# Performance work log

Hardware: AMD Instinct MI355X
Metric: run time of the kernel (lower is better)

Reference implementation:

```python
import jax, jax.numpy as jnp
import numpy as np
import math


def setup_inputs() -> dict:
    key = jax.random.key(0)
    kq, kk, kv = jax.random.split(key, 3)
    B, HQ, HKV, S, D = 1, 32, 8, 2048, 128
    query = jax.random.normal(kq, (B, HQ, S, D), dtype=jnp.float32)
    key_s = jax.random.normal(kk, (B, HKV, S, D), dtype=jnp.float32)
    value = jax.random.normal(kv, (B, HKV, S, D), dtype=jnp.float32)
    # additive causal mask [B,1,S,S]: 0 where j<=i, large-negative elsewhere
    neg = jnp.finfo(jnp.float32).min
    i = jnp.arange(S)
    attention_mask = jnp.where(i[None, :] <= i[:, None], 0.0, neg).astype(jnp.float32)[None, None]
    return {"query": query, "key": key_s, "value": value,
            "attention_mask": attention_mask, "window_size": 1024}


def reference(query, key, value, attention_mask, window_size):
    B, HQ, S, D = query.shape
    groups = HQ // key.shape[1]
    scaling = 1.0 / math.sqrt(D)
    # repeat_kv (GQA -> MHA)
    k = jnp.repeat(key, groups, axis=1)   # [B,HQ,S,D]
    v = jnp.repeat(value, groups, axis=1)
    # ---- eager_attention_forward ----
    scores = jnp.einsum('bhqd,bhkd->bhqk', query, k) * scaling
    scores = scores + attention_mask[:, :, :, :S]
    attn_weights = jax.nn.softmax(scores.astype(jnp.float32), axis=-1).astype(query.dtype)
    attn_output = jnp.einsum('bhqk,bhkd->bhqd', attn_weights, v)
    attn_output = attn_output.transpose(0, 2, 1, 3)  # [B,S,HQ,D]
    # ---- compute_window_attn_weights ----
    W = window_size
    qw = query[:, :, -W:, :]                                  # [B,HQ,W,D]
    ww = jnp.einsum('bhqd,bhkd->bhqk', qw, k) / math.sqrt(D)  # [B,HQ,W,S]
    neg = jnp.finfo(ww.dtype).min
    r = jnp.arange(W)
    win_mask = jnp.where(r[None, :] <= r[:, None], 0.0, neg).astype(ww.dtype)  # [W,W]
    ww = ww.at[:, :, :, -W:].add(win_mask[None, None])
    window_attn_weights = jax.nn.softmax(ww.astype(jnp.float32), axis=-1).astype(query.dtype)
    return (attn_output, attn_weights, window_attn_weights)
```

## Files before the change

kernel.cpp:

```cpp
#include <hip/hip_runtime.h>
#include <hip/hip_bf16.h>

typedef __bf16 bf16x8 __attribute__((ext_vector_type(8)));
typedef float f32x4 __attribute__((ext_vector_type(4)));
static_assert(sizeof(bf16x8) == 16, "bf16x8 must be 16B");

constexpr int S = 2048, D = 128, HQ = 32, W = 1024;
constexpr float SCALE_L2E = 0.08838834764831845f * 1.4426950408889634f;

constexpr size_t O1 = (size_t)S * HQ * D;
constexpr size_t O2 = O1 + (size_t)HQ * S * S;
constexpr int TILE64 = 64 * 256;
constexpr int TILE32 = 32 * 256;

__device__ __forceinline__ void gl_lds16(const void* g, void* l) {
    __builtin_amdgcn_global_load_lds(
        (const __attribute__((address_space(1))) void*)(unsigned long long)g,
        (__attribute__((address_space(3))) void*)(unsigned int)(unsigned long long)l,
        16, 0, 0);
}
__device__ __forceinline__ void st4(float* p, f32x4 v) {
    *reinterpret_cast<f32x4*>(p) = v;
}

__global__ __launch_bounds__(256)
void prep_kernel(const float* __restrict__ K, const float* __restrict__ V,
                 char* __restrict__ KbI, char* __restrict__ VtI)
{
    __shared__ __attribute__((aligned(16))) __bf16 Vs[128][72];
    const int b = blockIdx.x, hkv = b >> 5, kt = b & 31;
    const int tid = threadIdx.x;
    const float* Ks   = K + ((size_t)hkv * S + kt * 64) * D;
    const float* Vsrc = V + ((size_t)hkv * S + kt * 64) * D;
    char* Kimg = KbI + (size_t)(hkv * 32 + kt) * TILE64;
    char* Vimg = VtI + (size_t)(hkv * 32 + kt) * TILE64;

    #pragma unroll
    for (int i = 0; i < 4; ++i) {
        int idx = tid + i * 256;
        int r = idx >> 4, sl = idx & 15;
        float4 a = *reinterpret_cast<const float4*>(Ks + r * D + sl * 8);
        float4 c = *reinterpret_cast<const float4*>(Ks + r * D + sl * 8 + 4);
        bf16x8 f = {(__bf16)a.x, (__bf16)a.y, (__bf16)a.z, (__bf16)a.w,
                    (__bf16)c.x, (__bf16)c.y, (__bf16)c.z, (__bf16)c.w};
        *reinterpret_cast<bf16x8*>(Kimg + r * 256 + ((sl * 16) ^ ((r & 7) << 4))) = f;
    }
    #pragma unroll
    for (int i = 0; i < 8; ++i) {
        int idx = tid + i * 256;
        int r = idx >> 5, c = (idx & 31) * 4;
        float4 vv = *reinterpret_cast<const float4*>(Vsrc + r * D + c);
        Vs[c + 0][r] = (__bf16)vv.x; Vs[c + 1][r] = (__bf16)vv.y;
        Vs[c + 2][r] = (__bf16)vv.z; Vs[c + 3][r] = (__bf16)vv.w;
    }
    __syncthreads();
    #pragma unroll
    for (int i = 0; i < 4; ++i) {
        int idx = tid + i * 256;
        int img = idx >> 9;
        int rem = idx & 511;
        int d = rem >> 2, sl = rem & 3;
        bf16x8 v = *reinterpret_cast<const bf16x8*>(&Vs[d][img * 32 + sl * 8]);
        *reinterpret_cast<bf16x8*>(Vimg + img * TILE32 + d * 64 + ((sl * 16) ^ ((d & 3) << 4))) = v;
    }
}

__global__ __launch_bounds__(256, 4)
void lsum_kernel(const float* __restrict__ Q, const char* __restrict__ KbI,
                 float* __restrict__ lsr)
{
    __shared__ __attribute__((aligned(16))) char BUF[2][TILE64];

    const int bid = blockIdx.x;
    const int j   = bid >> 5;
    const int qt = (j < 8) ? (16 + j) : (j < 16) ? (23 - j) : (j < 24) ? (47 - j) : (j - 24);
    const int b5 = bid & 31;
    const int h  = (b5 & 7) * 4 + (b5 >> 3);
    const int hkv = h >> 2;
    const int tid = threadIdx.x, wave = tid >> 6, lane = tid & 63;
    const int lo = lane & 15, hi = lane >> 4;
    const int qw0 = (qt << 6) + wave * 16;

    const char* Ktiles = KbI + (size_t)hkv * 32 * TILE64;
    const float* Qh = Q + (size_t)h * S * D;

    bf16x8 qf[4];
    {
        const float* qs = Qh + (size_t)(qw0 + lo) * D + hi * 8;
        #pragma unroll
        for (int dc = 0; dc < 4; ++dc) {
            float4 a = *reinterpret_cast<const float4*>(qs + dc * 32);
            float4 b = *reinterpret_cast<const float4*>(qs + dc * 32 + 4);
            bf16x8 f;
            f[0] = (__bf16)(a.x * SCALE_L2E); f[1] = (__bf16)(a.y * SCALE_L2E);
            f[2] = (__bf16)(a.z * SCALE_L2E); f[3] = (__bf16)(a.w * SCALE_L2E);
            f[4] = (__bf16)(b.x * SCALE_L2E); f[5] = (__bf16)(b.y * SCALE_L2E);
            f[6] = (__bf16)(b.z * SCALE_L2E); f[7] = (__bf16)(b.w * SCALE_L2E);
            qf[dc] = f;
        }
    }

    float lsum[4] = {0.f, 0.f, 0.f, 0.f};
    {
        #pragma unroll
        for (int i = 0; i < 4; ++i)
            gl_lds16(Ktiles + (wave * 4 + i) * 1024 + lane * 16,
                     &BUF[0][0] + (wave * 4 + i) * 1024);
        __builtin_amdgcn_sched_barrier(0);
        asm volatile("s_waitcnt vmcnt(0)" ::: "memory");
        __builtin_amdgcn_s_barrier();
        __builtin_amdgcn_sched_barrier(0);

        int cur = 0;
        for (int kt = 0; kt <= qt; ++kt) {
            if (kt < qt) {
                const char* src = Ktiles + (size_t)(kt + 1) * TILE64;
                char* dst = &BUF[cur ^ 1][0];
                #pragma unroll
                for (int i = 0; i < 4; ++i)
                    gl_lds16(src + (wave * 4 + i) * 1024 + lane * 16, dst + (wave * 4 + i) * 1024);
                __builtin_amdgcn_sched_barrier(0);
            }
            const char* KtB = &BUF[cur][0];
            #pragma unroll
            for (int cg = 0; cg < 4; ++cg) {
                f32x4 acc = {0.f, 0.f, 0.f, 0.f};
                const int row = cg * 16 + lo, swzr = (row & 7) << 4;
                #pragma unroll
                for (int dc = 0; dc < 4; ++dc) {
                    bf16x8 kf = *reinterpret_cast<const bf16x8*>(
                        KtB + row * 256 + ((hi * 16 + dc * 64) ^ swzr));
                    acc = __builtin_amdgcn_mfma_f32_16x16x32_bf16(qf[dc], kf, acc, 0, 0, 0);
                }
                const int k = (kt << 6) + cg * 16 + lo;
                #pragma unroll
                for (int r = 0; r < 4; ++r) {
                    int q = qw0 + hi * 4 + r;
                    lsum[r] += (k <= q) ? exp2f(acc[r]) : 0.f;
                }
            }
            __builtin_amdgcn_sched_barrier(0);
            asm volatile("s_waitcnt vmcnt(0) lgkmcnt(0)" ::: "memory");
            __builtin_amdgcn_s_barrier();
            __builtin_amdgcn_sched_barrier(0);
            cur ^= 1;
        }
    }
    #pragma unroll
    for (int r = 0; r < 4; ++r) {
        float v = lsum[r];
        v += __shfl_xor(v, 1); v += __shfl_xor(v, 2);
        v += __shfl_xor(v, 4); v += __shfl_xor(v, 8);
        if (lo == 0) lsr[h * S + qw0 + hi * 4 + r] = 1.0f / v;
    }
}

__global__ __launch_bounds__(256, 4)
void attn_main(const float* __restrict__ Q, const char* __restrict__ KbI,
               const char* __restrict__ VtI, const float* __restrict__ lsr,
               float* __restrict__ out)
{
    __shared__ __attribute__((aligned(16))) char BUF[4][TILE32];
    __shared__ __attribute__((aligned(16))) char PST[4][1024];

    const int bid = blockIdx.x;
    const int j   = bid >> 5;
    const int qt = (j < 8) ? (16 + j) : (j < 16) ? (23 - j) : (j < 24) ? (47 - j) : (j - 24);
    const int b5 = bid & 31;
    const int h  = (b5 & 7) * 4 + (b5 >> 3);
    const int hkv = h >> 2;
    const int q0  = qt << 6;
    const int tid = threadIdx.x, wave = tid >> 6, lane = tid & 63;
    const int lo = lane & 15, hi = lane >> 4;
    const int qw0 = q0 + wave * 16;
    const bool winw = (qt >= 16);

    const char* Ktiles = KbI + (size_t)hkv * 32 * TILE64;
    const char* Vtiles = VtI + (size_t)hkv * 32 * TILE64;
    const float* Qh = Q + (size_t)h * S * D;

    bf16x8 qf[4];
    {
        const float* qs = Qh + (size_t)(qw0 + lo) * D + hi * 8;
        #pragma unroll
        for (int dc = 0; dc < 4; ++dc) {
            float4 a = *reinterpret_cast<const float4*>(qs + dc * 32);
            float4 b = *reinterpret_cast<const float4*>(qs + dc * 32 + 4);
            bf16x8 f;
            f[0] = (__bf16)(a.x * SCALE_L2E); f[1] = (__bf16)(a.y * SCALE_L2E);
            f[2] = (__bf16)(a.z * SCALE_L2E); f[3] = (__bf16)(a.w * SCALE_L2E);
            f[4] = (__bf16)(b.x * SCALE_L2E); f[5] = (__bf16)(b.y * SCALE_L2E);
            f[6] = (__bf16)(b.z * SCALE_L2E); f[7] = (__bf16)(b.w * SCALE_L2E);
            qf[dc] = f;
        }
    }
    float rcp_[4];
    {
        float4 rc = *reinterpret_cast<const float4*>(lsr + h * S + qw0 + hi * 4);
        rcp_[0] = rc.x; rcp_[1] = rc.y; rcp_[2] = rc.z; rcp_[3] = rc.w;
    }

    f32x4 oacc[8];
    #pragma unroll
    for (int i = 0; i < 8; ++i) oacc[i] = (f32x4){0.f, 0.f, 0.f, 0.f};
    char* Ps = PST[wave];
    const int nk32 = (qt + 1) * 2;

    {
        #pragma unroll
        for (int i = 0; i < 2; ++i) {
            gl_lds16(Ktiles + (wave * 2 + i) * 1024 + lane * 16, &BUF[0][0] + (wave * 2 + i) * 1024);
            gl_lds16(Vtiles + (wave * 2 + i) * 1024 + lane * 16, &BUF[2][0] + (wave * 2 + i) * 1024);
        }
        __builtin_amdgcn_sched_barrier(0);
        asm volatile("s_waitcnt vmcnt(0)" ::: "memory");
        __builtin_amdgcn_s_barrier();
        __builtin_amdgcn_sched_barrier(0);
    }

    int cur = 0;
    for (int t = 0; t < nk32; ++t) {
        const bool more = (t + 1 < nk32);
        if (more) {
            const char* sk = Ktiles + (size_t)(t + 1) * TILE32;
            const char* sv = Vtiles + (size_t)(t + 1) * TILE32;
            char* dk = &BUF[cur ^ 1][0];
            char* dv = &BUF[2 + (cur ^ 1)][0];
            #pragma unroll
            for (int i = 0; i < 2; ++i) {
                gl_lds16(sk + (wave * 2 + i) * 1024 + lane * 16, dk + (wave * 2 + i) * 1024);
                gl_lds16(sv + (wave * 2 + i) * 1024 + lane * 16, dv + (wave * 2 + i) * 1024);
            }
            __builtin_amdgcn_sched_barrier(0);
        }
        const char* KtB = &BUF[cur][0];
        const char* VtB = &BUF[2 + cur][0];
        const int kbase = t * 32;

        #pragma unroll
        for (int cg = 0; cg < 2; ++cg) {
            f32x4 acc = {0.f, 0.f, 0.f, 0.f};
            const int row = cg * 16 + lo, swzr = (row & 7) << 4;
            #pragma unroll
            for (int dc = 0; dc < 4; ++dc) {
                bf16x8 kf = *reinterpret_cast<const bf16x8*>(
                    KtB + row * 256 + ((hi * 16 + dc * 64) ^ swzr));
                acc = __builtin_amdgcn_mfma_f32_16x16x32_bf16(qf[dc], kf, acc, 0, 0, 0);
            }
            const int k = kbase + cg * 16 + lo;
            #pragma unroll
            for (int r = 0; r < 4; ++r) {
                const int q = qw0 + hi * 4 + r;
                float pv = (k <= q) ? exp2f(acc[r]) * rcp_[r] : 0.f;
                const int prow = hi * 4 + r;
                *reinterpret_cast<__bf16*>(
                    Ps + prow * 64 + ((2 * (cg * 16 + lo)) ^ ((prow & 3) << 4))) = (__bf16)pv;
            }
        }

        {
            const int row = lane >> 2;
            const int sl  = lane & 3;
            const int q = qw0 + row;
            bf16x8 pv8 = *reinterpret_cast<const bf16x8*>(
                Ps + row * 64 + ((sl * 16) ^ ((row & 3) << 4)));
            f32x4 f0 = {(float)pv8[0], (float)pv8[1], (float)pv8[2], (float)pv8[3]};
            f32x4 f1 = {(float)pv8[4], (float)pv8[5], (float)pv8[6], (float)pv8[7]};
            float* dstP = out + O1 + ((size_t)h * S + q) * S + kbase + sl * 8;
            st4(dstP, f0);
            st4(dstP + 4, f1);
            if (winw) {
                float* dstW = out + O2 + ((size_t)h * W + (q - W)) * S + kbase + sl * 8;
                st4(dstW, f0);
                st4(dstW + 4, f1);
            }
        }

        {
            bf16x8 pf = *reinterpret_cast<const bf16x8*>(
                Ps + lo * 64 + ((hi * 16) ^ ((lo & 3) << 4)));
            #pragma unroll
            for (int dg = 0; dg < 8; ++dg) {
                const int d = dg * 16 + lo;
                bf16x8 vf = *reinterpret_cast<const bf16x8*>(
                    VtB + d * 64 + ((hi * 16) ^ ((d & 3) << 4)));
                oacc[dg] = __builtin_amdgcn_mfma_f32_16x16x32_bf16(pf, vf, oacc[dg], 0, 0, 0);
            }
        }

        if (more) {
            __builtin_amdgcn_sched_barrier(0);
            if (winw) asm volatile("s_waitcnt vmcnt(4) lgkmcnt(0)" ::: "memory");
            else      asm volatile("s_waitcnt vmcnt(2) lgkmcnt(0)" ::: "memory");
            __builtin_amdgcn_s_barrier();
            __builtin_amdgcn_sched_barrier(0);
        }
        cur ^= 1;
    }

    {
        const int zr = lane >> 2;
        const int c0 = (lane & 3) * 16;
        const f32x4 z = {0.f, 0.f, 0.f, 0.f};
        const int q = qw0 + zr;
        for (int kt = qt + 1; kt < 32; ++kt) {
            float* dp = out + O1 + ((size_t)h * S + q) * S + kt * 64 + c0;
            #pragma unroll
            for (int jj = 0; jj < 4; ++jj) st4(dp + jj * 4, z);
            if (winw) {
                float* dw = out + O2 + ((size_t)h * W + (q - W)) * S + kt * 64 + c0;
                #pragma unroll
                for (int jj = 0; jj < 4; ++jj) st4(dw + jj * 4, z);
            }
        }
    }

    #pragma unroll
    for (int dg = 0; dg < 8; ++dg) {
        #pragma unroll
        for (int r = 0; r < 4; ++r) {
            const int q = qw0 + hi * 4 + r;
            out[((size_t)q * HQ + h) * D + dg * 16 + lo] = oacc[dg][r];
        }
    }
}

extern "C" void kernel_launch(void* const* d_in, const int* in_sizes, int n_in,
                              void* d_out, int out_size, void* d_ws, size_t ws_size,
                              hipStream_t stream)
{
    const float* Q = (const float*)d_in[0];
    const float* K = (const float*)d_in[1];
    const float* V = (const float*)d_in[2];
    float* out = (float*)d_out;

    char*  KbI = (char*)d_ws;
    char*  VtI = (char*)d_ws + (size_t)4 * 1024 * 1024;
    float* lsr = (float*)((char*)d_ws + (size_t)8 * 1024 * 1024);

    hipLaunchKernelGGL(prep_kernel, dim3(256),  dim3(256), 0, stream, K, V, KbI, VtI);
    hipLaunchKernelGGL(lsum_kernel, dim3(1024), dim3(256), 0, stream, Q, KbI, lsr);
    hipLaunchKernelGGL(attn_main,   dim3(1024), dim3(256), 0, stream, Q, KbI, VtI, lsr, out);
}
```

Measured before the change: 306.3 us.

## Drop LDS staging for K/V, read directly from global; move zero-fill to lsum kernel

Removes the global_load_lds double-buffered staging of K and V tiles in both kernels; each wave now loads its MFMA operands straight from global memory (L2-resident bf16 images), which also eliminates the block barriers. The zero-filling of the masked upper-triangle outputs moves from attn_main into lsum_kernel to balance work. The probability matrix is now written with scalar per-element stores instead of coalesced 32-byte vector stores from LDS, and the P staging buffer is double-buffered per wave. This trades LDS traffic and synchronization for redundant global/L2 reads and less coalesced output writes.

Measured after the change: 620.9 us. +102.7%, slower.

```diff
diff --git a/kernel.cpp b/kernel.cpp
--- a/kernel.cpp
+++ b/kernel.cpp
@@ -13,12 +13,6 @@
 constexpr int TILE64 = 64 * 256;
 constexpr int TILE32 = 32 * 256;
 
-__device__ __forceinline__ void gl_lds16(const void* g, void* l) {
-    __builtin_amdgcn_global_load_lds(
-        (const __attribute__((address_space(1))) void*)(unsigned long long)g,
-        (__attribute__((address_space(3))) void*)(unsigned int)(unsigned long long)l,
-        16, 0, 0);
-}
 __device__ __forceinline__ void st4(float* p, f32x4 v) {
     *reinterpret_cast<f32x4*>(p) = v;
 }
@@ -67,10 +61,8 @@
 
 __global__ __launch_bounds__(256, 4)
 void lsum_kernel(const float* __restrict__ Q, const char* __restrict__ KbI,
-                 float* __restrict__ lsr)
-{
-    __shared__ __attribute__((aligned(16))) char BUF[2][TILE64];
-
+                 float* __restrict__ lsr, float* __restrict__ out)
+{
     const int bid = blockIdx.x;
     const int j   = bid >> 5;
     const int qt = (j < 8) ? (16 + j) : (j < 16) ? (23 - j) : (j < 24) ? (47 - j) : (j - 24);
@@ -80,6 +72,7 @@
     const int tid = threadIdx.x, wave = tid >> 6, lane = tid & 63;
     const int lo = lane & 15, hi = lane >> 4;
     const int qw0 = (qt << 6) + wave * 16;
+    const bool winw = (qt >= 16);
 
     const char* Ktiles = KbI + (size_t)hkv * 32 * TILE64;
     const float* Qh = Q + (size_t)h * S * D;
@@ -101,49 +94,27 @@
     }
 
     float lsum[4] = {0.f, 0.f, 0.f, 0.f};
-    {
-        #pragma unroll
-        for (int i = 0; i < 4; ++i)
-            gl_lds16(Ktiles + (wave * 4 + i) * 1024 + lane * 16,
-                     &BUF[0][0] + (wave * 4 + i) * 1024);
-        __builtin_amdgcn_sched_barrier(0);
-        asm volatile("s_waitcnt vmcnt(0)" ::: "memory");
-        __builtin_amdgcn_s_barrier();
-        __builtin_amdgcn_sched_barrier(0);
-
-        int cur = 0;
-        for (int kt = 0; kt <= qt; ++kt) {
-            if (kt < qt) {
-                const char* src = Ktiles + (size_t)(kt + 1) * TILE64;
-                char* dst = &BUF[cur ^ 1][0];
-                #pragma unroll
-                for (int i = 0; i < 4; ++i)
-                    gl_lds16(src + (wave * 4 + i) * 1024 + lane * 16, dst + (wave * 4 + i) * 1024);
-                __builtin_amdgcn_sched_barrier(0);
-            }
-            const char* KtB = &BUF[cur][0];
-            #pragma unroll
-            for (int cg = 0; cg < 4; ++cg) {
-                f32x4 acc = {0.f, 0.f, 0.f, 0.f};
-                const int row = cg * 16 + lo, swzr = (row & 7) << 4;
-                #pragma unroll
-                for (int dc = 0; dc < 4; ++dc) {
-                    bf16x8 kf = *reinterpret_cast<const bf16x8*>(
-                        KtB + row * 256 + ((hi * 16 + dc * 64) ^ swzr));
-                    acc = __builtin_amdgcn_mfma_f32_16x16x32_bf16(qf[dc], kf, acc, 0, 0, 0);
-                }
-                const int k = (kt << 6) + cg * 16 + lo;
-                #pragma unroll
-                for (int r = 0; r < 4; ++r) {
-                    int q = qw0 + hi * 4 + r;
-                    lsum[r] += (k <= q) ? exp2f(acc[r]) : 0.f;
-                }
-            }
-            __builtin_amdgcn_sched_barrier(0);
-            asm volatile("s_waitcnt vmcnt(0) lgkmcnt(0)" ::: "memory");
-            __builtin_amdgcn_s_barrier();
-            __builtin_amdgcn_sched_barrier(0);
-            cur ^= 1;
+    for (int kt = 0; kt <= qt; ++kt) {
+        const char* Kt = Ktiles + (size_t)kt * TILE64;
+        #pragma unroll
+        for (int cg = 0; cg < 4; ++cg) {
+            const int row = cg * 16 + lo, swzr = (row & 7) << 4;
+            const char* rp = Kt + row * 256;
+            bf16x8 kf0 = *reinterpret_cast<const bf16x8*>(rp + ((hi * 16 +   0) ^ swzr));
+            bf16x8 kf1 = *reinterpret_cast<const bf16x8*>(rp + ((hi * 16 +  64) ^ swzr));
+            bf16x8 kf2 = *reinterpret_cast<const bf16x8*>(rp + ((hi * 16 + 128) ^ swzr));
+            bf16x8 kf3 = *reinterpret_cast<const bf16x8*>(rp + ((hi * 16 + 192) ^ swzr));
+            f32x4 acc = {0.f, 0.f, 0.f, 0.f};
+            acc = __builtin_amdgcn_mfma_f32_16x16x32_bf16(qf[0], kf0, acc, 0, 0, 0);
+            acc = __builtin_amdgcn_mfma_f32_16x16x32_bf16(qf[1], kf1, acc, 0, 0, 0);
+            acc = __builtin_amdgcn_mfma_f32_16x16x32_bf16(qf[2], kf2, acc, 0, 0, 0);
+            acc = __builtin_amdgcn_mfma_f32_16x16x32_bf16(qf[3], kf3, acc, 0, 0, 0);
+            const int k = (kt << 6) + cg * 16 + lo;
+            #pragma unroll
+            for (int r = 0; r < 4; ++r) {
+                int q = qw0 + hi * 4 + r;
+                lsum[r] += (k <= q) ? exp2f(acc[r]) : 0.f;
+            }
         }
     }
     #pragma unroll
@@ -153,6 +124,23 @@
         v += __shfl_xor(v, 4); v += __shfl_xor(v, 8);
         if (lo == 0) lsr[h * S + qw0 + hi * 4 + r] = 1.0f / v;
     }
+
+    {
+        const int zr = lane >> 2;
+        const int c0 = (lane & 3) * 16;
+        const f32x4 z = {0.f, 0.f, 0.f, 0.f};
+        const int q = qw0 + zr;
+        for (int kt = qt + 1; kt < 32; ++kt) {
+            float* dp = out + O1 + ((size_t)h * S + q) * S + kt * 64 + c0;
+            #pragma unroll
+            for (int jj = 0; jj < 4; ++jj) st4(dp + jj * 4, z);
+            if (winw) {
+                float* dw = out + O2 + ((size_t)h * W + (q - W)) * S + kt * 64 + c0;
+                #pragma unroll
+                for (int jj = 0; jj < 4; ++jj) st4(dw + jj * 4, z);
+            }
+        }
+    }
 }
 
 __global__ __launch_bounds__(256, 4)
@@ -160,8 +148,7 @@
                const char* __restrict__ VtI, const float* __restrict__ lsr,
                float* __restrict__ out)
 {
-    __shared__ __attribute__((aligned(16))) char BUF[4][TILE32];
-    __shared__ __attribute__((aligned(16))) char PST[4][1024];
+    __shared__ __attribute__((aligned(16))) char PST[4][2][1024];
 
     const int bid = blockIdx.x;
     const int j   = bid >> 5;
@@ -169,10 +156,9 @@
     const int b5 = bid & 31;
     const int h  = (b5 & 7) * 4 + (b5 >> 3);
     const int hkv = h >> 2;
-    const int q0  = qt << 6;
     const int tid = threadIdx.x, wave = tid >> 6, lane = tid & 63;
     const int lo = lane & 15, hi = lane >> 4;
-    const int qw0 = q0 + wave * 16;
+    const int qw0 = (qt << 6) + wave * 16;
     const bool winw = (qt >= 16);
 
     const char* Ktiles = KbI + (size_t)hkv * 32 * TILE64;
@@ -203,50 +189,27 @@
     f32x4 oacc[8];
     #pragma unroll
     for (int i = 0; i < 8; ++i) oacc[i] = (f32x4){0.f, 0.f, 0.f, 0.f};
-    char* Ps = PST[wave];
     const int nk32 = (qt + 1) * 2;
 
-    {
-        #pragma unroll
-        for (int i = 0; i < 2; ++i) {
-            gl_lds16(Ktiles + (wave * 2 + i) * 1024 + lane * 16, &BUF[0][0] + (wave * 2 + i) * 1024);
-            gl_lds16(Vtiles + (wave * 2 + i) * 1024 + lane * 16, &BUF[2][0] + (wave * 2 + i) * 1024);
-        }
-        __builtin_amdgcn_sched_barrier(0);
-        asm volatile("s_waitcnt vmcnt(0)" ::: "memory");
-        __builtin_amdgcn_s_barrier();
-        __builtin_amdgcn_sched_barrier(0);
-    }
-
-    int cur = 0;
     for (int t = 0; t < nk32; ++t) {
-        const bool more = (t + 1 < nk32);
-        if (more) {
-            const char* sk = Ktiles + (size_t)(t + 1) * TILE32;
-            const char* sv = Vtiles + (size_t)(t + 1) * TILE32;
-            char* dk = &BUF[cur ^ 1][0];
-            char* dv = &BUF[2 + (cur ^ 1)][0];
-            #pragma unroll
-            for (int i = 0; i < 2; ++i) {
-                gl_lds16(sk + (wave * 2 + i) * 1024 + lane * 16, dk + (wave * 2 + i) * 1024);
-                gl_lds16(sv + (wave * 2 + i) * 1024 + lane * 16, dv + (wave * 2 + i) * 1024);
-            }
-            __builtin_amdgcn_sched_barrier(0);
-        }
-        const char* KtB = &BUF[cur][0];
-        const char* VtB = &BUF[2 + cur][0];
+        const char* Kt = Ktiles + (size_t)t * TILE32;
+        const char* Vt = Vtiles + (size_t)t * TILE32;
+        char* Ps = PST[wave][t & 1];
         const int kbase = t * 32;
 
         #pragma unroll
         for (int cg = 0; cg < 2; ++cg) {
+            const int row = cg * 16 + lo, swzr = (row & 7) << 4;
+            const char* rp = Kt + row * 256;
+            bf16x8 kf0 = *reinterpret_cast<const bf16x8*>(rp + ((hi * 16 +   0) ^ swzr));
+            bf16x8 kf1 = *reinterpret_cast<const bf16x8*>(rp + ((hi * 16 +  64) ^ swzr));
+            bf16x8 kf2 = *reinterpret_cast<const bf16x8*>(rp + ((hi * 16 + 128) ^ swzr));
+            bf16x8 kf3 = *reinterpret_cast<const bf16x8*>(rp + ((hi * 16 + 192) ^ swzr));
             f32x4 acc = {0.f, 0.f, 0.f, 0.f};
-            const int row = cg * 16 + lo, swzr = (row & 7) << 4;
-            #pragma unroll
-            for (int dc = 0; dc < 4; ++dc) {
-                bf16x8 kf = *reinterpret_cast<const bf16x8*>(
-                    KtB + row * 256 + ((hi * 16 + dc * 64) ^ swzr));
-                acc = __builtin_amdgcn_mfma_f32_16x16x32_bf16(qf[dc], kf, acc, 0, 0, 0);
-            }
+            acc = __builtin_amdgcn_mfma_f32_16x16x32_bf16(qf[0], kf0, acc, 0, 0, 0);
+            acc = __builtin_amdgcn_mfma_f32_16x16x32_bf16(qf[1], kf1, acc, 0, 0, 0);
+            acc = __builtin_amdgcn_mfma_f32_16x16x32_bf16(qf[2], kf2, acc, 0, 0, 0);
+            acc = __builtin_amdgcn_mfma_f32_16x16x32_bf16(qf[3], kf3, acc, 0, 0, 0);
             const int k = kbase + cg * 16 + lo;
             #pragma unroll
             for (int r = 0; r < 4; ++r) {
@@ -255,24 +218,9 @@
                 const int prow = hi * 4 + r;
                 *reinterpret_cast<__bf16*>(
                     Ps + prow * 64 + ((2 * (cg * 16 + lo)) ^ ((prow & 3) << 4))) = (__bf16)pv;
-            }
-        }
-
-        {
-            const int row = lane >> 2;
-            const int sl  = lane & 3;
-            const int q = qw0 + row;
-            bf16x8 pv8 = *reinterpret_cast<const bf16x8*>(
-                Ps + row * 64 + ((sl * 16) ^ ((row & 3) << 4)));
-            f32x4 f0 = {(float)pv8[0], (float)pv8[1], (float)pv8[2], (float)pv8[3]};
-            f32x4 f1 = {(float)pv8[4], (float)pv8[5], (float)pv8[6], (float)pv8[7]};
-            float* dstP = out + O1 + ((size_t)h * S + q) * S + kbase + sl * 8;
-            st4(dstP, f0);
-            st4(dstP + 4, f1);
-            if (winw) {
-                float* dstW = out + O2 + ((size_t)h * W + (q - W)) * S + kbase + sl * 8;
-                st4(dstW, f0);
-                st4(dstW + 4, f1);
+                out[O1 + ((size_t)h * S + q) * S + k] = pv;
+                if (winw)
+                    out[O2 + ((size_t)h * W + (q - W)) * S + k] = pv;
             }
         }
 
@@ -283,34 +231,8 @@
             for (int dg = 0; dg < 8; ++dg) {
                 const int d = dg * 16 + lo;
                 bf16x8 vf = *reinterpret_cast<const bf16x8*>(
-                    VtB + d * 64 + ((hi * 16) ^ ((d & 3) << 4)));
+                    Vt + d * 64 + ((hi * 16) ^ ((d & 3) << 4)));
                 oacc[dg] = __builtin_amdgcn_mfma_f32_16x16x32_bf16(pf, vf, oacc[dg], 0, 0, 0);
-            }
-        }
-
-        if (more) {
-            __builtin_amdgcn_sched_barrier(0);
-            if (winw) asm volatile("s_waitcnt vmcnt(4) lgkmcnt(0)" ::: "memory");
-            else      asm volatile("s_waitcnt vmcnt(2) lgkmcnt(0)" ::: "memory");
-            __builtin_amdgcn_s_barrier();
-            __builtin_amdgcn_sched_barrier(0);
-        }
-        cur ^= 1;
-    }
-
-    {
-        const int zr = lane >> 2;
-        const int c0 = (lane & 3) * 16;
-        const f32x4 z = {0.f, 0.f, 0.f, 0.f};
-        const int q = qw0 + zr;
-        for (int kt = qt + 1; kt < 32; ++kt) {
-            float* dp = out + O1 + ((size_t)h * S + q) * S + kt * 64 + c0;
-            #pragma unroll
-            for (int jj = 0; jj < 4; ++jj) st4(dp + jj * 4, z);
-            if (winw) {
-                float* dw = out + O2 + ((size_t)h * W + (q - W)) * S + kt * 64 + c0;
-                #pragma unroll
-                for (int jj = 0; jj < 4; ++jj) st4(dw + jj * 4, z);
             }
         }
     }
@@ -339,6 +261,6 @@
     float* lsr = (float*)((char*)d_ws + (size_t)8 * 1024 * 1024);
 
     hipLaunchKernelGGL(prep_kernel, dim3(256),  dim3(256), 0, stream, K, V, KbI, VtI);
-    hipLaunchKernelGGL(lsum_kernel, dim3(1024), dim3(256), 0, stream, Q, KbI, lsr);
+    hipLaunchKernelGGL(lsum_kernel, dim3(1024), dim3(256), 0, stream, Q, KbI, lsr, out);
     hipLaunchKernelGGL(attn_main,   dim3(1024), dim3(256), 0, stream, Q, KbI, VtI, lsr, out);
 }
```
